# Performance work log

Measured on AMD Instinct MI355X. Metric: run time of the kernel, lower is better.

The kernel has to match this reference:

```python
import jax, jax.numpy as jnp
import numpy as np

H, L, N = 512, 4096, 64

def make_dplr_hippo(n):
    # HiPPO-LegS -> NPLR -> DPLR diagonalization (numpy, init-time only)
    p0 = np.sqrt(1 + 2 * np.arange(n))
    A = p0[:, None] * p0[None, :]
    A = -(np.tril(A) - np.diag(np.arange(n)))
    p = np.sqrt(np.arange(n) + 0.5)
    b = np.sqrt(2 * np.arange(n) + 1.0)
    S = A + p[:, None] * p[None, :]
    Lambda_re = np.full(n, np.diagonal(S).mean())
    Lambda_im, V = np.linalg.eigh(S * -1j)
    Pc = V.conj().T @ p
    Bc = V.conj().T @ b
    return Lambda_re, Lambda_im, Pc, Bc

def setup_inputs() -> dict:
    key = jax.random.key(0)
    k_u, k_c, k_s = jax.random.split(key, 3)
    lr, li, Pc, Bc = make_dplr_hippo(N)
    tile = lambda v: jnp.tile(jnp.asarray(v, jnp.float32)[None, :], (H, 1))
    dt_min, dt_max = 0.001, 0.1
    log_step = (jax.random.uniform(k_s, (H, 1), jnp.float32)
                * (np.log(dt_max) - np.log(dt_min)) + np.log(dt_min))
    return {
        "u": jax.random.normal(k_u, (H, L), jnp.float32),
        "Lambda_re": tile(lr), "Lambda_im": tile(li),
        "P_re": tile(Pc.real), "P_im": tile(Pc.imag),
        "B_re": tile(Bc.real), "B_im": tile(Bc.imag),
        "C": jax.random.normal(k_c, (H, N, 2), jnp.float32) * (0.5 ** 0.5),
        "D": jnp.ones((H, 1), jnp.float32),
        "log_step": log_step,
    }

def reference(u, Lambda_re, Lambda_im, P_re, P_im, B_re, B_im, C, D, log_step):
    # u: [H, L]; all params leading dim H (vmapped channels)
    Lam = jnp.minimum(Lambda_re, -1e-4) + 1j * Lambda_im      # [H, N]
    P = P_re + 1j * P_im                                       # [H, N]
    B = B_re + 1j * B_im                                       # [H, N]
    Cc = C[..., 0] + 1j * C[..., 1]                             # [H, N]
    step = jnp.exp(log_step)                                    # [H, 1]
    Lseq = u.shape[-1]
    Omega = jnp.exp(-2j * jnp.pi * (jnp.arange(Lseq) / Lseq)).astype(jnp.complex64)  # [L]
    g = (2.0 / step) * ((1.0 - Omega) / (1.0 + Omega))[None, :]  # [H, L]
    c = 2.0 / (1.0 + Omega)                                      # [L]
    denom = 1.0 / (g[:, :, None] - Lam[:, None, :])              # [H, L, N]
    cauchy = lambda v: jnp.einsum('hn,hln->hl', v, denom)
    k00 = cauchy(Cc.conj() * B)
    k01 = cauchy(Cc.conj() * P)
    k10 = cauchy(P.conj() * B)
    k11 = cauchy(P.conj() * P)
    atRoots = c[None, :] * (k00 - k01 * (1.0 / (1.0 + k11)) * k10)
    K = jnp.fft.ifft(atRoots, Lseq, axis=-1).real                # [H, L] conv kernel
    # causal convolution via zero-padded FFT (length 2L)
    ud = jnp.fft.rfft(u, n=2 * Lseq, axis=-1)
    Kd = jnp.fft.rfft(K, n=2 * Lseq, axis=-1)
    y = jnp.fft.irfft(ud * Kd, n=2 * Lseq, axis=-1)[..., :Lseq]
    return y + D * u
```

## Files before the change

kernel.cpp:

```cpp
#include <hip/hip_runtime.h>
#include <math.h>

#define NT 512

typedef float v2 __attribute__((ext_vector_type(2)));

__device__ __forceinline__ v2 vrot(v2 a){ return (v2){-a.y, a.x}; }
__device__ __forceinline__ v2 vconj(v2 a){ return (v2){a.x, -a.y}; }
__device__ __forceinline__ v2 vcmul(v2 a, v2 b){ return a.x*b + a.y*vrot(b); }
__device__ __forceinline__ v2 vfma1(float s, v2 v, v2 acc){
    return (v2){ __builtin_fmaf(s, v.x, acc.x), __builtin_fmaf(s, v.y, acc.y) };
}

__device__ __forceinline__ int SW(int e){ return e ^ (((e>>5) ^ (e>>9)) & 15); }

__device__ __forceinline__ int d8r4(int x){
    return ((x&7)<<9) | (((x>>3)&7)<<6) | (((x>>6)&7)<<3) | ((x>>9)&7);
}
__device__ __forceinline__ int rev3(int t){
    return ((t&7)<<6) | (t&56) | ((t>>6)&7);
}

__device__ __forceinline__ void dft8_inv(v2 t[8], v2 y[8]) {
    const float RH = 0.70710678f;
    v2 p  = t[0]+t[4], m  = t[0]-t[4], q  = t[2]+t[6], r  = t[2]-t[6];
    v2 rr = vrot(r);
    v2 E0 = p+q, E2 = p-q, E1 = m+rr, E3 = m-rr;
    v2 p2 = t[1]+t[5], m2 = t[1]-t[5], q2 = t[3]+t[7], r2 = t[3]-t[7];
    v2 rr2 = vrot(r2);
    v2 O0 = p2+q2, O2 = p2-q2, O1 = m2+rr2, O3 = m2-rr2;
    v2 W1O = RH*(O1 + vrot(O1));
    v2 W2O = vrot(O2);
    v2 W3O = vrot(RH*(O3 + vrot(O3)));
    y[0] = E0 + O0;  y[4] = E0 - O0;
    y[1] = E1 + W1O; y[5] = E1 - W1O;
    y[2] = E2 + W2O; y[6] = E2 - W2O;
    y[3] = E3 + W3O; y[7] = E3 - W3O;
}

__device__ __forceinline__ void dft8_fwd(v2 t[8], v2 y[8]) {
    const float RH = 0.70710678f;
    v2 p  = t[0]+t[4], m  = t[0]-t[4], q  = t[2]+t[6], r  = t[2]-t[6];
    v2 rr = vrot(r);
    v2 E0 = p+q, E2 = p-q, E1 = m-rr, E3 = m+rr;
    v2 p2 = t[1]+t[5], m2 = t[1]-t[5], q2 = t[3]+t[7], r2 = t[3]-t[7];
    v2 rr2 = vrot(r2);
    v2 O0 = p2+q2, O2 = p2-q2, O1 = m2-rr2, O3 = m2+rr2;
    v2 W1O = RH*(O1 - vrot(O1));
    v2 W2O = (v2){O2.y, -O2.x};
    v2 W3O = (-RH)*(O3 + vrot(O3));
    y[0] = E0 + O0;  y[4] = E0 - O0;
    y[1] = E1 + W1O; y[5] = E1 - W1O;
    y[2] = E2 + W2O; y[6] = E2 - W2O;
    y[3] = E3 + W3O; y[7] = E3 - W3O;
}

__device__ __forceinline__ void apply_tw_inv(v2 t[8], float fm, int j) {
    float sb, cb; __sincosf(fm*(float)j, &sb, &cb);
    v2 W1 = (v2){cb, sb};
    v2 W2 = vcmul(W1,W1), W3 = vcmul(W1,W2), W4 = vcmul(W2,W2),
       W5 = vcmul(W2,W3), W6 = vcmul(W3,W3), W7 = vcmul(W3,W4);
    t[1]=vcmul(t[1],W1); t[2]=vcmul(t[2],W2); t[3]=vcmul(t[3],W3);
    t[4]=vcmul(t[4],W4); t[5]=vcmul(t[5],W5); t[6]=vcmul(t[6],W6);
    t[7]=vcmul(t[7],W7);
}

template<int Q>
__device__ __forceinline__ void r8_dit_inv(v2* buf, int tid) {
    int j = tid & (Q-1);
    int base = 8*tid - 7*j;
    v2 t[8];
    #pragma unroll
    for (int k = 0; k < 8; ++k) t[k] = buf[SW(base + k*Q)];
    apply_tw_inv(t, 6.2831853072f / (float)(8*Q), j);
    v2 y[8];
    dft8_inv(t, y);
    #pragma unroll
    for (int m = 0; m < 8; ++m) buf[SW(base + m*Q)] = y[m];
    __syncthreads();
}

template<int Q>
__device__ __forceinline__ void r8_dif_fwd(v2* buf, int tid) {
    int j = tid & (Q-1);
    int baseL = 8*tid - 7*j;
    v2 W1=(v2){1.0f,0.0f},W2=W1,W3=W1,W4=W1,W5=W1,W6=W1,W7=W1;
    if (Q > 1) {
        const float fm = -6.2831853072f / (float)(8*Q);
        float sb, cb; __sincosf(fm*(float)j, &sb, &cb);
        W1 = (v2){cb, sb};
        W2 = vcmul(W1,W1); W3 = vcmul(W1,W2); W4 = vcmul(W2,W2);
        W5 = vcmul(W2,W3); W6 = vcmul(W3,W3); W7 = vcmul(W3,W4);
    }
    #pragma unroll 1
    for (int hh = 0; hh < 2; ++hh) {
        int base = baseL + (hh << 12);
        v2 t[8];
        #pragma unroll
        for (int k = 0; k < 8; ++k) t[k] = buf[SW(base + k*Q)];
        v2 y[8];
        dft8_fwd(t, y);
        if (Q > 1) {
            y[1]=vcmul(y[1],W1); y[2]=vcmul(y[2],W2); y[3]=vcmul(y[3],W3);
            y[4]=vcmul(y[4],W4); y[5]=vcmul(y[5],W5); y[6]=vcmul(y[6],W6);
            y[7]=vcmul(y[7],W7);
        }
        #pragma unroll
        for (int m = 0; m < 8; ++m) buf[SW(base + m*Q)] = y[m];
    }
    __syncthreads();
}

__global__ void __launch_bounds__(64)
s4_prep(const float* __restrict__ Lre, const float* __restrict__ Lim,
        const float* __restrict__ Pre, const float* __restrict__ Pim,
        const float* __restrict__ Bre, const float* __restrict__ Bim,
        const float* __restrict__ Cin,
        float* __restrict__ ws8, float* __restrict__ ws1)
{
    int idx = blockIdx.x*64 + threadIdx.x;
    float lre = fminf(Lre[idx], -1e-4f);
    float lim = Lim[idx];
    float pr = Pre[idx], pi = Pim[idx];
    float br = Bre[idx], bi = Bim[idx];
    float cr = Cin[2*idx], ci = Cin[2*idx+1];
    v2 cc = (v2){cr, -ci};
    v2 w00 = vcmul(cc, (v2){br, bi});
    v2 w01 = vcmul(cc, (v2){pr, pi});
    v2 w10 = vcmul((v2){pr,-pi}, (v2){br, bi});
    float* o = ws8 + idx*8;
    o[0] = -lre;  o[1] = -lim;
    o[2] = w00.x; o[3] = w00.y;
    o[4] = w01.x; o[5] = w01.y;
    o[6] = w10.x; o[7] = w10.y;
    ws1[idx] = pr*pr + pi*pi;
}

__global__ void __launch_bounds__(NT)
s4_fused(const float* __restrict__ u,
         const float* __restrict__ Din, const float* __restrict__ logstep,
         const float* __restrict__ ws8, const float* __restrict__ ws1,
         float* __restrict__ out)
{
    __shared__ v2 buf[8192];
    const int tid = threadIdx.x;
    const int h = blockIdx.x;

    const float step = expf(logstep[h]);
    const float tos  = 2.0f / step;
    const float hstep = 0.5f * step;
    const float* pp = ws8 + (h*64)*8;
    const float* pw = ws1 + h*64;

    v2 a4[4];
    #pragma unroll 1
    for (int hp = 0; hp < 2; ++hp) {
        float tv[4];
        v2 cf[4], k00[4], k01[4], k10[4], k11[4];
        const int lbase = hp*(4*NT);
        #pragma unroll
        for (int i = 0; i < 4; ++i) {
            int l = lbase + i*NT + tid;
            float ang = -6.2831855f * ((float)l * (1.0f/4096.0f));
            float sh, ch; __sincosf(0.5f*ang, &sh, &ch);
            float traw = -tos * sh * __builtin_amdgcn_rcpf(ch);
            float t = fminf(fmaxf(traw, -1e18f), 1e18f);
            tv[i] = t;
            cf[i] = (v2){1.0f, t*hstep};
            k00[i]=(v2)(0.0f); k01[i]=(v2)(0.0f); k10[i]=(v2)(0.0f); k11[i]=(v2)(0.0f);
        }
        #pragma unroll 4
        for (int n = 0; n < 64; ++n) {
            float nlre = pp[n*8+0], nlim = pp[n*8+1];
            v2 w00 = (v2){pp[n*8+2], pp[n*8+3]};
            v2 w01 = (v2){pp[n*8+4], pp[n*8+5]};
            v2 w10 = (v2){pp[n*8+6], pp[n*8+7]};
            float w11r = pw[n];
            float lre2 = nlre*nlre;
            #pragma unroll
            for (int i = 0; i < 4; ++i) {
                float s = tv[i] + nlim;
                float inv = __builtin_amdgcn_rcpf(__builtin_fmaf(s, s, lre2));
                v2 p = (v2){nlre, s} * inv;
                v2 cp = (v2){p.x, -p.y};
                v2 rp = (v2){p.y,  p.x};
                k00[i] = vfma1(w00.y, rp, vfma1(w00.x, cp, k00[i]));
                k01[i] = vfma1(w01.y, rp, vfma1(w01.x, cp, k01[i]));
                k10[i] = vfma1(w10.y, rp, vfma1(w10.x, cp, k10[i]));
                k11[i] = vfma1(w11r,  cp, k11[i]);
            }
        }
        #pragma unroll
        for (int i = 0; i < 4; ++i) {
            v2 opk = (v2){1.0f + k11[i].x, k11[i].y};
            float iv = __builtin_amdgcn_rcpf(opk.x*opk.x + opk.y*opk.y);
            v2 r11 = vconj(opk) * iv;
            v2 t  = vcmul(vcmul(k01[i], r11), k10[i]);
            v2 res = vcmul(cf[i], k00[i] - t);
            if (hp == 0) buf[SW(tid + 512*i)] = res;
            else         a4[i] = res;
        }
    }
    {
        v2 t[8];
        #pragma unroll
        for (int k = 0; k < 4; ++k) t[k] = buf[SW(tid + 512*k)];
        #pragma unroll
        for (int k = 0; k < 4; ++k) t[4+k] = a4[k];
        __syncthreads();
        v2 y[8];
        dft8_inv(t, y);
        int tb8 = 8*rev3(tid);
        #pragma unroll
        for (int m = 0; m < 8; ++m) buf[SW(tb8 + m)] = y[m];
    }
    __syncthreads();

    r8_dit_inv<8 >(buf, tid);
    r8_dit_inv<64>(buf, tid);

    {
        v2 t[8];
        #pragma unroll
        for (int k = 0; k < 8; ++k) t[k] = buf[SW(tid + 512*k)];
        apply_tw_inv(t, 6.2831853072f / 4096.0f, tid);
        v2 y[8];
        dft8_inv(t, y);
        float uval[8];
        const float* up = u + h*4096;
        #pragma unroll
        for (int m = 0; m < 8; ++m) uval[m] = up[tid + 512*m];
        __syncthreads();
        float s2, c2; __sincosf(-6.2831853072f/8192.0f*(float)tid, &s2, &c2);
        v2 cur = (v2){c2, s2};
        const v2 C16n = (v2){0.92387953f, -0.38268343f};
        #pragma unroll
        for (int m = 0; m < 8; ++m) {
            int l = tid + 512*m;
            v2 z = (v2){uval[m], y[m].x * (1.0f/4096.0f)};
            buf[SW(l)]      = z;
            buf[SW(l+4096)] = vcmul(z, cur);
            cur = vcmul(cur, C16n);
        }
    }
    __syncthreads();

    r8_dif_fwd<512>(buf, tid);
    r8_dif_fwd<64 >(buf, tid);
    r8_dif_fwd<8  >(buf, tid);
    r8_dif_fwd<1  >(buf, tid);

    {
        float sb, cb; __sincosf(6.2831853072f/8192.0f*(float)tid, &sb, &cb);
        v2 cur = (v2){cb, sb};
        const v2 C16p = (v2){0.92387953f, 0.38268343f};
        v2 v[8];
        #pragma unroll 1
        for (int i = 0; i < 8; ++i) {
            int r  = i*NT + tid;
            int k1 = r,        k1c = (8192 - r) & 8191;
            int k2 = r + 4096, k2c = 4096 - r;
            v2 za = buf[SW(((k1 &1)<<12) + d8r4(k1 >>1))];
            v2 zb = buf[SW(((k1c&1)<<12) + d8r4(k1c>>1))];
            v2 zc = buf[SW(((k2 &1)<<12) + d8r4(k2 >>1))];
            v2 zd = buf[SW(((k2c&1)<<12) + d8r4(k2c>>1))];
            v2 U1 = 0.5f*(za + vconj(zb));
            v2 K1 = -0.5f*vrot(za - vconj(zb));
            v2 Yr = vcmul(U1, K1);
            v2 U2 = 0.5f*(zc + vconj(zd));
            v2 K2 = -0.5f*vrot(zc - vconj(zd));
            v2 Ys = vcmul(U2, K2);
            v[i] = (Yr + Ys) + vrot(vcmul(cur, Yr - Ys));
            cur = vcmul(cur, C16p);
        }
        __syncthreads();
        v2 y[8];
        dft8_inv(v, y);
        int tb8 = 8*rev3(tid);
        #pragma unroll
        for (int m = 0; m < 8; ++m) buf[SW(tb8 + m)] = y[m];
    }
    __syncthreads();

    r8_dit_inv<8 >(buf, tid);
    r8_dit_inv<64>(buf, tid);

    {
        v2 t[8];
        #pragma unroll
        for (int k = 0; k < 8; ++k) t[k] = buf[SW(tid + 512*k)];
        apply_tw_inv(t, 6.2831853072f / 4096.0f, tid);
        v2 y[8];
        dft8_inv(t, y);
        const float Dh = Din[h];
        const float sc = 1.0f / 8192.0f;
        const v2* u2 = (const v2*)(u + h*4096);
        v2*     out2 = (v2*)(out + h*4096);
        #pragma unroll
        for (int m = 0; m < 4; ++m) {
            int n = tid + 512*m;
            out2[n] = sc*y[m] + Dh*u2[n];
        }
    }
}

extern "C" void kernel_launch(void* const* d_in, const int* in_sizes, int n_in,
                              void* d_out, int out_size, void* d_ws, size_t ws_size,
                              hipStream_t stream)
{
    const float* u       = (const float*)d_in[0];
    const float* Lre     = (const float*)d_in[1];
    const float* Lim     = (const float*)d_in[2];
    const float* Pre     = (const float*)d_in[3];
    const float* Pim     = (const float*)d_in[4];
    const float* Bre     = (const float*)d_in[5];
    const float* Bim     = (const float*)d_in[6];
    const float* Cin     = (const float*)d_in[7];
    const float* Din     = (const float*)d_in[8];
    const float* logstep = (const float*)d_in[9];
    float* out = (float*)d_out;
    const int H = in_sizes[8];

    float* ws8 = (float*)d_ws;
    float* ws1 = ws8 + (size_t)H*64*8;

    hipLaunchKernelGGL(s4_prep, dim3(H), dim3(64), 0, stream,
                       Lre, Lim, Pre, Pim, Bre, Bim, Cin, ws8, ws1);
    hipLaunchKernelGGL(s4_fused, dim3(H), dim3(NT), 0, stream,
                       u, Din, logstep, ws8, ws1, out);
}
```

Measured before the change: 162.4 us.

## Fuse first forward FFT stage into registers and use wave barriers for intra-wave stages

The first radix-8 DIF stage of the 8192-point forward FFT is now computed in registers, directly after building the zero-padded and twiddled input. This removes one LDS write/read round trip and a block barrier. Block-wide __syncthreads between FFT stages whose data exchange stays inside one 64-thread wavefront (Q=8→64, Q=64→8→1) are replaced with wave barriers. The redundant barrier before the in-place register write-back is also dropped. Correctness now depends on those stage access patterns staying wave-local.

Result: no change. 159.7 us (-1.6%).

```diff
diff --git a/kernel.cpp b/kernel.cpp
--- a/kernel.cpp
+++ b/kernel.cpp
@@ -65,7 +65,8 @@
     t[7]=vcmul(t[7],W7);
 }
 
-template<int Q>
+
+template<int Q, bool BAR>
 __device__ __forceinline__ void r8_dit_inv(v2* buf, int tid) {
     int j = tid & (Q-1);
     int base = 8*tid - 7*j;
@@ -77,10 +78,11 @@
     dft8_inv(t, y);
     #pragma unroll
     for (int m = 0; m < 8; ++m) buf[SW(base + m*Q)] = y[m];
-    __syncthreads();
-}
-
-template<int Q>
+    if (BAR) __syncthreads();
+    else     __builtin_amdgcn_wave_barrier();
+}
+
+template<int Q, bool BAR>
 __device__ __forceinline__ void r8_dif_fwd(v2* buf, int tid) {
     int j = tid & (Q-1);
     int baseL = 8*tid - 7*j;
@@ -108,7 +110,8 @@
         #pragma unroll
         for (int m = 0; m < 8; ++m) buf[SW(base + m*Q)] = y[m];
     }
-    __syncthreads();
+    if (BAR) __syncthreads();
+    else     __builtin_amdgcn_wave_barrier();
 }
 
 __global__ void __launch_bounds__(64)
@@ -216,8 +219,8 @@
     }
     __syncthreads();
 
-    r8_dit_inv<8 >(buf, tid);
-    r8_dit_inv<64>(buf, tid);
+    r8_dit_inv<8,  false>(buf, tid);
+    r8_dit_inv<64, true >(buf, tid);
 
     {
         v2 t[8];
@@ -230,25 +233,41 @@
         const float* up = u + h*4096;
         #pragma unroll
         for (int m = 0; m < 8; ++m) uval[m] = up[tid + 512*m];
-        __syncthreads();
         float s2, c2; __sincosf(-6.2831853072f/8192.0f*(float)tid, &s2, &c2);
-        v2 cur = (v2){c2, s2};
+        v2 cur0 = (v2){c2, s2};
         const v2 C16n = (v2){0.92387953f, -0.38268343f};
-        #pragma unroll
-        for (int m = 0; m < 8; ++m) {
-            int l = tid + 512*m;
-            v2 z = (v2){uval[m], y[m].x * (1.0f/4096.0f)};
-            buf[SW(l)]      = z;
-            buf[SW(l+4096)] = vcmul(z, cur);
-            cur = vcmul(cur, C16n);
-        }
+        v2 zL[8], zU[8];
+        {
+            v2 cur = cur0;
+            #pragma unroll
+            for (int k = 0; k < 8; ++k) {
+                zL[k] = (v2){uval[k], y[k].x * (1.0f/4096.0f)};
+                zU[k] = vcmul(zL[k], cur);
+                cur = vcmul(cur, C16n);
+            }
+        }
+        v2 V1 = vcmul(cur0, cur0);
+        v2 V2 = vcmul(V1,V1), V3 = vcmul(V1,V2), V4 = vcmul(V2,V2),
+           V5 = vcmul(V2,V3), V6 = vcmul(V3,V3), V7 = vcmul(V3,V4);
+        v2 s[8];
+        dft8_fwd(zL, s);
+        s[1]=vcmul(s[1],V1); s[2]=vcmul(s[2],V2); s[3]=vcmul(s[3],V3);
+        s[4]=vcmul(s[4],V4); s[5]=vcmul(s[5],V5); s[6]=vcmul(s[6],V6);
+        s[7]=vcmul(s[7],V7);
+        #pragma unroll
+        for (int m = 0; m < 8; ++m) buf[SW(tid + 512*m)] = s[m];
+        dft8_fwd(zU, s);
+        s[1]=vcmul(s[1],V1); s[2]=vcmul(s[2],V2); s[3]=vcmul(s[3],V3);
+        s[4]=vcmul(s[4],V4); s[5]=vcmul(s[5],V5); s[6]=vcmul(s[6],V6);
+        s[7]=vcmul(s[7],V7);
+        #pragma unroll
+        for (int m = 0; m < 8; ++m) buf[SW(4096 + tid + 512*m)] = s[m];
     }
     __syncthreads();
 
-    r8_dif_fwd<512>(buf, tid);
-    r8_dif_fwd<64 >(buf, tid);
-    r8_dif_fwd<8  >(buf, tid);
-    r8_dif_fwd<1  >(buf, tid);
+    r8_dif_fwd<64, false>(buf, tid);
+    r8_dif_fwd<8,  false>(buf, tid);
+    r8_dif_fwd<1,  true >(buf, tid);
 
     {
         float sb, cb; __sincosf(6.2831853072f/8192.0f*(float)tid, &sb, &cb);
@@ -282,8 +301,8 @@
     }
     __syncthreads();
 
-    r8_dit_inv<8 >(buf, tid);
-    r8_dit_inv<64>(buf, tid);
+    r8_dit_inv<8,  false>(buf, tid);
+    r8_dit_inv<64, true >(buf, tid);
 
     {
         v2 t[8];
```
